# Optimization experiments

Measured on AMD Instinct MI355X. Metric: run time of the kernel, lower is better.

The kernel has to match this reference:

```python
import jax, jax.numpy as jnp
import numpy as np

N = 20000   # nodes
E = 240000  # edges (avg degree 12)
D = 128     # hidden_dim
H = 4       # heads
C = D // H  # head dim = 32
L = 3       # layers


def _ln(x, g, b):
    m = x.mean(-1, keepdims=True)
    v = ((x - m) ** 2).mean(-1, keepdims=True)
    return (x - m) / jnp.sqrt(v + 1e-5) * g + b


def setup_inputs() -> dict:
    key = jax.random.key(0)
    ks = iter(jax.random.split(key, 64))
    def w(shape, s=0.02):
        return jax.random.normal(next(ks), shape, jnp.float32) * s
    z = lambda shape: jnp.zeros(shape, jnp.float32)
    o = lambda shape: jnp.ones(shape, jnp.float32)
    inp = {
        'xyz': jax.random.normal(next(ks), (N, 3), jnp.float32) * 10.0,
        'attr': jax.random.uniform(next(ks), (N, 1), jnp.float32),
        'edge_index': jax.random.randint(next(ks), (2, E), 0, N, jnp.int32),
        # input encoder
        'enc_W': w((4, D)), 'enc_b': z((D,)), 'enc_g': o((D,)), 'enc_bb': z((D,)),
        # relative position MLP
        'pos_W1': w((3, D)), 'pos_b1': z((D,)), 'pos_g': o((D,)), 'pos_bb': z((D,)),
        'pos_W2': w((D, D)), 'pos_b2': z((D,)),
        # TransformerConv per-layer params (stacked over L)
        'Wq': w((L, D, D)), 'bq': z((L, D)),
        'Wk': w((L, D, D)), 'bk': z((L, D)),
        'Wv': w((L, D, D)), 'bv': z((L, D)),
        'We': w((L, D, D)),                 # lin_edge (no bias in PyG)
        'Wskip': w((L, D, D)), 'bskip': z((L, D)),
        'Wbeta': w((L, 3 * D, 1)),          # lin_beta (no bias)
        'ln1_g': o((L, D)), 'ln1_b': z((L, D)),
        'ln2_g': o((L, D)), 'ln2_b': z((L, D)),
        'fW1': w((L, D, 2 * D)), 'fb1': z((L, 2 * D)),
        'fW2': w((L, 2 * D, D)), 'fb2': z((L, D)),
        # heads
        'cls_W1': w((D, D // 2)), 'cls_b1': z((D // 2,)),
        'cls_W2': w((D // 2, 4)), 'cls_b2': z((4,)),
        'box_W1': w((D, D // 2)), 'box_b1': z((D // 2,)),
        'box_W2': w((D // 2, 7)), 'box_b2': z((7,)),
    }
    return inp


def reference(xyz, attr, edge_index, enc_W, enc_b, enc_g, enc_bb,
              pos_W1, pos_b1, pos_g, pos_bb, pos_W2, pos_b2,
              Wq, bq, Wk, bk, Wv, bv, We, Wskip, bskip, Wbeta,
              ln1_g, ln1_b, ln2_g, ln2_b, fW1, fb1, fW2, fb2,
              cls_W1, cls_b1, cls_W2, cls_b2, box_W1, box_b1, box_W2, box_b2):
    n = xyz.shape[0]
    src, dst = edge_index[0], edge_index[1]  # x_j = x[src], x_i = x[dst]; aggregate at dst
    inv_sqrt_c = 1.0 / float(np.sqrt(C))

    # input encoder: Linear -> LayerNorm -> ReLU
    x = jnp.concatenate([xyz, attr], axis=-1)
    x = jax.nn.relu(_ln(x @ enc_W + enc_b, enc_g, enc_bb))

    # relative position encoding per edge: i, j = edge_index; rel = xyz[j] - xyz[i]
    rel = xyz[dst] - xyz[src]
    e = jax.nn.relu(_ln(rel @ pos_W1 + pos_b1, pos_g, pos_bb)) @ pos_W2 + pos_b2  # [E, D]

    for l in range(L):
        # TransformerConv (beta=True, concat=True, edge_dim=D), eval mode (no dropout)
        q = (x @ Wq[l] + bq[l]).reshape(n, H, C)
        k = (x @ Wk[l] + bk[l]).reshape(n, H, C)
        v = (x @ Wv[l] + bv[l]).reshape(n, H, C)
        ee = (e @ We[l]).reshape(-1, H, C)          # [E, H, C]
        kj = k[src] + ee                             # edge-conditioned keys
        alpha = (q[dst] * kj).sum(-1) * inv_sqrt_c   # [E, H]
        amax = jax.ops.segment_max(alpha, dst, num_segments=n)
        ex = jnp.exp(alpha - amax[dst])
        den = jax.ops.segment_sum(ex, dst, num_segments=n)
        a = ex / den[dst]                            # scatter softmax over in-edges of dst
        msg = (v[src] + ee) * a[:, :, None]
        out = jax.ops.segment_sum(msg, dst, num_segments=n).reshape(n, D)
        # beta-gated skip
        r = x @ Wskip[l] + bskip[l]
        beta = jax.nn.sigmoid(jnp.concatenate([out, r, out - r], axis=-1) @ Wbeta[l])  # [N,1]
        out = beta * r + (1.0 - beta) * out
        # residual + LN + FFN + residual + LN
        x = _ln(out + x, ln1_g[l], ln1_b[l])
        h = jax.nn.gelu(x @ fW1[l] + fb1[l], approximate=False) @ fW2[l] + fb2[l]
        x = _ln(h + x, ln2_g[l], ln2_b[l])

    cls_logits = jax.nn.relu(x @ cls_W1 + cls_b1) @ cls_W2 + cls_b2  # [N, 4]
    box_pred = jax.nn.relu(x @ box_W1 + box_b1) @ box_W2 + box_b2    # [N, 7]
    return (cls_logits, box_pred)
```

## Files before the change

### kernel.cpp

```cpp
#include <hip/hip_runtime.h>
#include <hip/hip_bf16.h>
#include <math.h>

#define DD 128

typedef __attribute__((ext_vector_type(8))) short short8;
typedef __attribute__((ext_vector_type(4))) float f32x4;


__device__ __forceinline__ unsigned short f2b(float f) {
    unsigned u = __float_as_uint(f);
    return (unsigned short)((u + 0x7FFFu + ((u >> 16) & 1u)) >> 16);
}
__device__ __forceinline__ float b2f(unsigned short b) {
    return __uint_as_float(((unsigned)b) << 16);
}
__device__ __forceinline__ unsigned packbf(float a, float b) {
    return (unsigned)f2b(a) | ((unsigned)f2b(b) << 16);
}

__device__ __forceinline__ void redsum2_128(float& a, float& b) {
    #pragma unroll
    for (int off = 32; off > 0; off >>= 1) {
        a += __shfl_down(a, off);
        b += __shfl_down(b, off);
    }
    __shared__ float sa[2], sb[2];
    int w = threadIdx.x >> 6;
    if ((threadIdx.x & 63) == 0) { sa[w] = a; sb[w] = b; }
    __syncthreads();
    a = sa[0] + sa[1];
    b = sb[0] + sb[1];
    __syncthreads();
}


__global__ void packw12_kernel(const float* __restrict__ Wq, const float* __restrict__ Wk,
                               const float* __restrict__ Wv, const float* __restrict__ Ws,
                               unsigned* __restrict__ Wp) {
    int bid = blockIdx.x, y = blockIdx.y, d = threadIdx.x;
    int l = y >> 2, wt = y & 3;
    const float* W = (wt == 0 ? Wq : wt == 1 ? Wk : wt == 2 ? Wv : Ws) + (size_t)l * DD * DD;
    float w0 = W[(size_t)(2 * bid) * DD + d];
    float w1 = W[(size_t)(2 * bid + 1) * DD + d];
    Wp[y * 8192 + (((d << 6) + bid) ^ ((d & 7) << 2))] = packbf(w0, w1);
}

__global__ void wcombp_kernel(const float* __restrict__ W2, const float* __restrict__ b2,
                              const float* __restrict__ We, unsigned* __restrict__ Wp,
                              float* __restrict__ b2We) {
    int bid = blockIdx.x, y = blockIdx.y, d = threadIdx.x;
    const float* We_l = We + (size_t)y * DD * DD;
    __shared__ float sa0[DD], sa1[DD];
    if (bid < 64) { sa0[d] = W2[(2 * bid) * DD + d]; sa1[d] = W2[(2 * bid + 1) * DD + d]; }
    else          { sa0[d] = b2[d]; sa1[d] = 0.f; }
    __syncthreads();
    float acc0 = 0.f, acc1 = 0.f;
    #pragma unroll 8
    for (int kk = 0; kk < DD; ++kk) {
        float w = We_l[kk * DD + d];
        acc0 += sa0[kk] * w;
        acc1 += sa1[kk] * w;
    }
    if (bid < 64) Wp[y * 8192 + (((d << 6) + bid) ^ ((d & 7) << 2))] = packbf(acc0, acc1);
    else          b2We[y * DD + d] = acc0;
}

struct B4 { const float* b[4]; };

__global__ __launch_bounds__(256) void proj_kernel(
        const unsigned short* __restrict__ xb, const unsigned* __restrict__ Wp4, B4 bias,
        unsigned short* __restrict__ qkv, float* __restrict__ rbuf, int rowsN, int rtN,
        const float4* __restrict__ rel4, const float* __restrict__ pw,
        const float* __restrict__ bbp, const unsigned* __restrict__ Wpee,
        const float* __restrict__ biasee, unsigned short* __restrict__ eeout,
        int rowsE, int rtE) {
    __shared__ unsigned Bt[8192];
    __shared__ float sc[640];
    const int t = threadIdx.x;
    const int lane = t & 63, wid = t >> 6;
    const int kqo = (lane >> 4) * 8;

    if ((int)blockIdx.x < rtE) {
        const int rowBase = (int)blockIdx.x << 6;
        #pragma unroll
        for (int i = 0; i < 8; ++i)
            *(uint4*)&Bt[(i * 256 + t) * 4] = *(const uint4*)&Wpee[(i * 256 + t) * 4];
        for (int i = t; i < 640; i += 256)
            sc[i] = (i < 512) ? pw[i] : bbp[i - 512];
        int arow = rowBase + wid * 16 + (lane & 15);
        if (arow > rowsE - 1) arow = rowsE - 1;
        float4 rv = rel4[arow];
        __syncthreads();
        short8 a[4];
        #pragma unroll
        for (int kc = 0; kc < 4; ++kc) {
            union { short8 s; unsigned short u[8]; } cv;
            #pragma unroll
            for (int j = 0; j < 8; ++j) {
                int d = kc * 32 + kqo + j;
                float y = fmaf(rv.x, sc[d], fmaf(rv.y, sc[128 + d], fmaf(rv.z, sc[256 + d], sc[384 + d])));
                cv.u[j] = f2b(fmaxf(fmaf(y, rv.w, sc[512 + d]), 0.f));
            }
            a[kc] = cv.s;
        }
        f32x4 acc[8];
        #pragma unroll
        for (int i = 0; i < 8; ++i) acc[i] = (f32x4){0.f, 0.f, 0.f, 0.f};
        #pragma unroll
        for (int ng = 0; ng < 8; ++ng) {
            int col = ng * 16 + (lane & 15);
            #pragma unroll
            for (int kc = 0; kc < 4; ++kc) {
                int kidx = kc * 16 + (lane >> 4) * 4;
                const short8 b = *(const short8*)((const char*)Bt +
                        ((((col << 6) + kidx) ^ ((col & 7) << 2)) << 2));
                acc[ng] = __builtin_amdgcn_mfma_f32_16x16x32_bf16(a[kc], b, acc[ng], 0, 0, 0);
            }
        }
        __syncthreads();
        unsigned short* sb16 = (unsigned short*)Bt;
        #pragma unroll
        for (int ng = 0; ng < 8; ++ng) {
            int col = ng * 16 + (lane & 15);
            float bv = biasee[col];
            int cp = col >> 1, cb = col & 1;
            #pragma unroll
            for (int r = 0; r < 4; ++r) {
                int row = wid * 16 + (lane >> 4) * 4 + r;
                sb16[((row << 6) + (cp ^ ((row & 7) << 2))) * 2 + cb] = f2b(acc[ng][r] + bv);
            }
        }
        __syncthreads();
        unsigned* outw = (unsigned*)eeout;
        #pragma unroll
        for (int i = 0; i < 4; ++i) {
            int j = i * 1024 + t * 4;
            int row = j >> 6, cp = j & 63;
            uint4 v = *(const uint4*)&Bt[(row << 6) + (cp ^ ((row & 7) << 2))];
            int grow = rowBase + row;
            if (grow < rowsE) *(uint4*)&outw[(size_t)grow * 64 + cp] = v;
        }
        return;
    }

    int bidx = (int)blockIdx.x - rtE;
    const int y = bidx / rtN;
    const int rowBase = (bidx % rtN) << 6;
    const unsigned* Wp = Wp4 + y * 8192;
    #pragma unroll
    for (int i = 0; i < 8; ++i)
        *(uint4*)&Bt[(i * 256 + t) * 4] = *(const uint4*)&Wp[(i * 256 + t) * 4];
    int arow = rowBase + wid * 16 + (lane & 15);
    if (arow > rowsN - 1) arow = rowsN - 1;
    short8 a[4];
    #pragma unroll
    for (int kc = 0; kc < 4; ++kc)
        a[kc] = *(const short8*)(xb + (size_t)arow * DD + kc * 32 + kqo);
    __syncthreads();
    f32x4 acc[8];
    #pragma unroll
    for (int i = 0; i < 8; ++i) acc[i] = (f32x4){0.f, 0.f, 0.f, 0.f};
    #pragma unroll
    for (int ng = 0; ng < 8; ++ng) {
        int col = ng * 16 + (lane & 15);
        #pragma unroll
        for (int kc = 0; kc < 4; ++kc) {
            int kidx = kc * 16 + (lane >> 4) * 4;
            const short8 b = *(const short8*)((const char*)Bt +
                    ((((col << 6) + kidx) ^ ((col & 7) << 2)) << 2));
            acc[ng] = __builtin_amdgcn_mfma_f32_16x16x32_bf16(a[kc], b, acc[ng], 0, 0, 0);
        }
    }
    const float* bs = bias.b[y];
    if (y == 3) {
        #pragma unroll
        for (int ng = 0; ng < 8; ++ng) {
            int col = ng * 16 + (lane & 15);
            float bv = bs[col];
            #pragma unroll
            for (int r = 0; r < 4; ++r) {
                int grow = rowBase + wid * 16 + (lane >> 4) * 4 + r;
                if (grow < rowsN) rbuf[(size_t)grow * DD + col] = acc[ng][r] + bv;
            }
        }
        return;
    }
    __syncthreads();
    unsigned short* sb16 = (unsigned short*)Bt;
    #pragma unroll
    for (int ng = 0; ng < 8; ++ng) {
        int col = ng * 16 + (lane & 15);
        float bv = bs[col];
        int cp = col >> 1, cb = col & 1;
        #pragma unroll
        for (int r = 0; r < 4; ++r) {
            int row = wid * 16 + (lane >> 4) * 4 + r;
            sb16[((row << 6) + (cp ^ ((row & 7) << 2))) * 2 + cb] = f2b(acc[ng][r] + bv);
        }
    }
    __syncthreads();
    unsigned* outw = (unsigned*)qkv;
    #pragma unroll
    for (int i = 0; i < 4; ++i) {
        int j = i * 1024 + t * 4;
        int row = j >> 6, cp = j & 63;
        uint4 v = *(const uint4*)&Bt[(row << 6) + (cp ^ ((row & 7) << 2))];
        int grow = rowBase + row;
        if (grow < rowsN) *(uint4*)&outw[(size_t)grow * 192 + (y << 6) + cp] = v;
    }
}

template <int ACT>
__global__ __launch_bounds__(256) void mgemm(
        const unsigned short* __restrict__ A, const float* __restrict__ W,
        const float* __restrict__ bias, unsigned short* __restrict__ out,
        int rows, int K, int Dout) {
    __shared__ unsigned Bt[8192];
    const int t = threadIdx.x;
    const int rowBase = blockIdx.x << 6;
    const int colBase = blockIdx.y << 7;
    const int lane = t & 63, wid = t >> 6;
    f32x4 acc[8];
    #pragma unroll
    for (int i = 0; i < 8; ++i) acc[i] = (f32x4){0.f, 0.f, 0.f, 0.f};
    int arow = rowBase + wid * 16 + (lane & 15);
    if (arow > rows - 1) arow = rows - 1;
    const int kqo = (lane >> 4) * 8;
    for (int k0 = 0; k0 < K; k0 += 128) {
        if (k0) __syncthreads();
        #pragma unroll 8
        for (int it = 0; it < 32; ++it) {
            int idx = it * 256 + t;
            int n = idx & 127, kp = idx >> 7;
            int krow = k0 + kp * 2;
            float w0 = W[(size_t)krow * Dout + colBase + n];
            float w1 = W[(size_t)(krow + 1) * Dout + colBase + n];
            Bt[((n << 6) + kp) ^ ((n & 7) << 2)] = packbf(w0, w1);
        }
        __syncthreads();
        short8 a[4];
        #pragma unroll
        for (int kc = 0; kc < 4; ++kc)
            a[kc] = *(const short8*)(A + (size_t)arow * K + k0 + kc * 32 + kqo);
        #pragma unroll
        for (int ng = 0; ng < 8; ++ng) {
            int col = ng * 16 + (lane & 15);
            #pragma unroll
            for (int kc = 0; kc < 4; ++kc) {
                int kidx = kc * 16 + (lane >> 4) * 4;
                const short8 b = *(const short8*)((const char*)Bt +
                        ((((col << 6) + kidx) ^ ((col & 7) << 2)) << 2));
                acc[ng] = __builtin_amdgcn_mfma_f32_16x16x32_bf16(a[kc], b, acc[ng], 0, 0, 0);
            }
        }
    }
    __syncthreads();
    unsigned short* sb16 = (unsigned short*)Bt;
    #pragma unroll
    for (int ng = 0; ng < 8; ++ng) {
        int col = ng * 16 + (lane & 15);
        float bv = bias[colBase + col];
        int cp = col >> 1, cb = col & 1;
        #pragma unroll
        for (int r = 0; r < 4; ++r) {
            int row = wid * 16 + (lane >> 4) * 4 + r;
            float val = acc[ng][r] + bv;
            if (ACT == 1) val = 0.5f * val * (1.f + erff(val * 0.70710678118654752f));
            else if (ACT == 2) val = fmaxf(val, 0.f);
            sb16[((row << 6) + (cp ^ ((row & 7) << 2))) * 2 + cb] = f2b(val);
        }
    }
    __syncthreads();
    unsigned* outw = (unsigned*)out;
    const int strideU = Dout >> 1, cbU = colBase >> 1;
    #pragma unroll
    for (int i = 0; i < 4; ++i) {
        int j = i * 1024 + t * 4;
        int row = j >> 6, cp = j & 63;
        uint4 v = *(const uint4*)&Bt[(row << 6) + (cp ^ ((row & 7) << 2))];
        int grow = rowBase + row;
        if (grow < rows) *(uint4*)&outw[(size_t)grow * strideU + cbU + cp] = v;
    }
}

__global__ __launch_bounds__(256) void ffn_fused(
        const unsigned short* __restrict__ xbin, const float* __restrict__ W1,
        const float* __restrict__ b1f, const float* __restrict__ W2,
        const float* __restrict__ b2f, const float* __restrict__ g,
        const float* __restrict__ bbn, float* __restrict__ x,
        unsigned short* __restrict__ xb, int rows) {
    __shared__ unsigned Bt[8192];
    __shared__ unsigned h1t[8192];
    const int t = threadIdx.x;
    const int rowBase = blockIdx.x << 6;
    const int lane = t & 63, wid = t >> 6;
    const int kqo = (lane >> 4) * 8;
    int arow = rowBase + wid * 16 + (lane & 15);
    if (arow > rows - 1) arow = rows - 1;

    short8 a[4];
    #pragma unroll
    for (int kc = 0; kc < 4; ++kc)
        a[kc] = *(const short8*)(xbin + (size_t)arow * DD + kc * 32 + kqo);

    unsigned short* h16 = (unsigned short*)h1t;
    for (int half = 0; half < 2; ++half) {
        if (half) __syncthreads();
        #pragma unroll 8
        for (int it = 0; it < 32; ++it) {
            int idx = it * 256 + t;
            int n = idx & 127, kp = idx >> 7;
            float w0 = W1[(size_t)(2 * kp) * 256 + half * 128 + n];
            float w1 = W1[(size_t)(2 * kp + 1) * 256 + half * 128 + n];
            Bt[((n << 6) + kp) ^ ((n & 7) << 2)] = packbf(w0, w1);
        }
        __syncthreads();
        f32x4 acc[8];
        #pragma unroll
        for (int i = 0; i < 8; ++i) acc[i] = (f32x4){0.f, 0.f, 0.f, 0.f};
        #pragma unroll
        for (int ng = 0; ng < 8; ++ng) {
            int col = ng * 16 + (lane & 15);
            #pragma unroll
            for (int kc = 0; kc < 4; ++kc) {
                int kidx = kc * 16 + (lane >> 4) * 4;
                const short8 b = *(const short8*)((const char*)Bt +
                        ((((col << 6) + kidx) ^ ((col & 7) << 2)) << 2));
                acc[ng] = __builtin_amdgcn_mfma_f32_16x16x32_bf16(a[kc], b, acc[ng], 0, 0, 0);
            }
        }
        #pragma unroll
        for (int ng = 0; ng < 8; ++ng) {
            int col = half * 128 + ng * 16 + (lane & 15);
            float bv = b1f[col];
            int cp = col >> 1, cb = col & 1;
            #pragma unroll
            for (int r = 0; r < 4; ++r) {
                int row = wid * 16 + (lane >> 4) * 4 + r;
                float val = acc[ng][r] + bv;
                val = 0.5f * val * (1.f + erff(val * 0.70710678118654752f));
                h16[((row << 7) + (cp ^ ((row & 7) << 2))) * 2 + cb] = f2b(val);
            }
        }
    }
    f32x4 accF[8];
    #pragma unroll
    for (int i = 0; i < 8; ++i) accF[i] = (f32x4){0.f, 0.f, 0.f, 0.f};
    const int lrow = wid * 16 + (lane & 15);
    for (int c = 0; c < 2; ++c) {
        __syncthreads();
        #pragma unroll 8
        for (int it = 0; it < 32; ++it) {
            int idx = it * 256 + t;
            int n = idx & 127, kp = idx >> 7;
            int krow = c * 128 + kp * 2;
            float w0 = W2[(size_t)krow * DD + n];
            float w1 = W2[(size_t)(krow + 1) * DD + n];
            Bt[((n << 6) + kp) ^ ((n & 7) << 2)] = packbf(w0, w1);
        }
        __syncthreads();
        short8 ah[4];
        #pragma unroll
        for (int kc = 0; kc < 4; ++kc) {
            int cp4 = c * 64 + kc * 16 + (lane >> 4) * 4;
            ah[kc] = *(const short8*)&h1t[(lrow << 7) + (cp4 ^ ((lrow & 7) << 2))];
        }
        #pragma unroll
        for (int ng = 0; ng < 8; ++ng) {
            int col = ng * 16 + (lane & 15);
            #pragma unroll
            for (int kc = 0; kc < 4; ++kc) {
                int kidx = kc * 16 + (lane >> 4) * 4;
                const short8 b = *(const short8*)((const char*)Bt +
                        ((((col << 6) + kidx) ^ ((col & 7) << 2)) << 2));
                accF[ng] = __builtin_amdgcn_mfma_f32_16x16x32_bf16(ah[kc], b, accF[ng], 0, 0, 0);
            }
        }
    }
    float tt[8][4];
    float rs[4] = {0.f, 0.f, 0.f, 0.f}, rs2[4] = {0.f, 0.f, 0.f, 0.f};
    #pragma unroll
    for (int ng = 0; ng < 8; ++ng) {
        int col = ng * 16 + (lane & 15);
        float bv = b2f[col];
        #pragma unroll
        for (int r = 0; r < 4; ++r) {
            int grow = rowBase + wid * 16 + (lane >> 4) * 4 + r;
            float xo = (grow < rows) ? x[(size_t)grow * DD + col] : 0.f;
            float v = accF[ng][r] + bv + xo;
            tt[ng][r] = v;
            rs[r] += v;
            rs2[r] += v * v;
        }
    }
    #pragma unroll
    for (int r = 0; r < 4; ++r) {
        #pragma unroll
        for (int m = 1; m < 16; m <<= 1) {
            rs[r] += __shfl_xor(rs[r], m);
            rs2[r] += __shfl_xor(rs2[r], m);
        }
    }
    __syncthreads();
    unsigned short* sb16 = (unsigned short*)Bt;
    #pragma unroll
    for (int ng = 0; ng < 8; ++ng) {
        int col = ng * 16 + (lane & 15);
        float gg = g[col], bbb = bbn[col];
        int cp = col >> 1, cb = col & 1;
        #pragma unroll
        for (int r = 0; r < 4; ++r) {
            int grow = rowBase + wid * 16 + (lane >> 4) * 4 + r;
            float mean = rs[r] * (1.f / DD);
            float var = rs2[r] * (1.f / DD) - mean * mean;
            float val = (tt[ng][r] - mean) * rsqrtf(var + 1e-5f) * gg + bbb;
            if (grow < rows) x[(size_t)grow * DD + col] = val;
            int row = wid * 16 + (lane >> 4) * 4 + r;
            sb16[((row << 6) + (cp ^ ((row & 7) << 2))) * 2 + cb] = f2b(val);
        }
    }
    __syncthreads();
    unsigned* outw = (unsigned*)xb;
    #pragma unroll
    for (int i = 0; i < 4; ++i) {
        int j = i * 1024 + t * 4;
        int row = j >> 6, cp = j & 63;
        uint4 v = *(const uint4*)&Bt[(row << 6) + (cp ^ ((row & 7) << 2))];
        int grow = rowBase + row;
        if (grow < rows) *(uint4*)&outw[(size_t)grow * 64 + cp] = v;
    }
}


__global__ void enc_kernel(const float* __restrict__ xyz, const float* __restrict__ attr,
                           const float* __restrict__ W, const float* __restrict__ b,
                           const float* __restrict__ g, const float* __restrict__ bb,
                           float* __restrict__ x, unsigned short* __restrict__ xb) {
    int i = blockIdx.x, d = threadIdx.x;
    __shared__ float sin4[4];
    if (d < 3) sin4[d] = xyz[i * 3 + d];
    if (d == 3) sin4[3] = attr[i];
    __syncthreads();
    float y = b[d];
    #pragma unroll
    for (int kk = 0; kk < 4; ++kk) y += sin4[kk] * W[kk * DD + d];
    float s = y, s2 = y * y;
    redsum2_128(s, s2);
    float mean = s * (1.0f / DD);
    float var = s2 * (1.0f / DD) - mean * mean;
    float xn = fmaxf((y - mean) * rsqrtf(var + 1e-5f) * g[d] + bb[d], 0.f);
    x[i * DD + d] = xn;
    xb[(size_t)i * DD + d] = f2b(xn);
}

__global__ void posprep_kernel(const float* __restrict__ W1, const float* __restrict__ b1,
                               const float* __restrict__ g, float* __restrict__ pw) {
    int d = threadIdx.x;
    float w0 = W1[d], w1 = W1[DD + d], w2 = W1[2 * DD + d], b = b1[d];
    float s0 = w0, s1 = w1;
    redsum2_128(s0, s1);
    float s2 = w2, s3 = b;
    redsum2_128(s2, s3);
    float c0 = w0 - s0 * (1.f / DD), c1 = w1 - s1 * (1.f / DD);
    float c2 = w2 - s2 * (1.f / DD), bc = b - s3 * (1.f / DD);
    float gd = g[d];
    pw[d] = c0 * gd; pw[DD + d] = c1 * gd; pw[2 * DD + d] = c2 * gd; pw[3 * DD + d] = bc * gd;
    float p0 = c0 * c0, p1 = c0 * c1; redsum2_128(p0, p1);
    float p2 = c0 * c2, p3 = c1 * c1; redsum2_128(p2, p3);
    float p4 = c1 * c2, p5 = c2 * c2; redsum2_128(p4, p5);
    float p6 = c0 * bc, p7 = c1 * bc; redsum2_128(p6, p7);
    float p8 = c2 * bc, p9 = bc * bc; redsum2_128(p8, p9);
    if (d == 0) {
        pw[512] = p0 * (1.f / DD); pw[513] = p1 * (1.f / DD); pw[514] = p2 * (1.f / DD);
        pw[515] = p3 * (1.f / DD); pw[516] = p4 * (1.f / DD); pw[517] = p5 * (1.f / DD);
        pw[518] = p6 * (1.f / DD); pw[519] = p7 * (1.f / DD); pw[520] = p8 * (1.f / DD);
        pw[521] = p9 * (1.f / DD);
    }
}


__global__ void hist_kernel(const int* __restrict__ ei, int* __restrict__ deg, int E) {
    int e = blockIdx.x * blockDim.x + threadIdx.x;
    if (e < E) atomicAdd(&deg[ei[E + e]], 1);
}

__global__ void scan_kernel(const int* __restrict__ deg, int* __restrict__ ptr, int n) {
    __shared__ int partial[1024];
    int t = threadIdx.x;
    int CH = (n + 1023) >> 10;
    int beg = t * CH;
    int end = beg + CH; if (end > n) end = n;
    int s = 0;
    for (int i = beg; i < end; ++i) s += deg[i];
    partial[t] = s;
    __syncthreads();
    for (int off = 1; off < 1024; off <<= 1) {
        int add = (t >= off) ? partial[t - off] : 0;
        __syncthreads();
        partial[t] += add;
        __syncthreads();
    }
    int base = (t == 0) ? 0 : partial[t - 1];
    for (int i = beg; i < end; ++i) {
        ptr[i] = base;
        base += deg[i];
    }
    if (end == n && beg < n) ptr[n] = base;
}

__global__ void scatter_kernel(const int* __restrict__ ei, const float* __restrict__ xyz,
                               const float* __restrict__ pw, const int* __restrict__ ptr,
                               int* __restrict__ cur, int* __restrict__ cs_src,
                               float4* __restrict__ rel4, int E) {
    int e = blockIdx.x * blockDim.x + threadIdx.x;
    if (e >= E) return;
    int srcn = ei[e], dstn = ei[E + e];
    int p = atomicAdd(&cur[dstn], 1);
    int slot = ptr[dstn] + p;
    cs_src[slot] = srcn;
    float r0 = xyz[dstn * 3]     - xyz[srcn * 3];
    float r1 = xyz[dstn * 3 + 1] - xyz[srcn * 3 + 1];
    float r2 = xyz[dstn * 3 + 2] - xyz[srcn * 3 + 2];
    float var = pw[512] * r0 * r0 + pw[515] * r1 * r1 + pw[517] * r2 * r2
              + 2.f * (pw[513] * r0 * r1 + pw[514] * r0 * r2 + pw[516] * r1 * r2)
              + 2.f * (pw[518] * r0 + pw[519] * r1 + pw[520] * r2) + pw[521];
    rel4[slot] = make_float4(r0, r1, r2, rsqrtf(var + 1e-5f));
}

__global__ __launch_bounds__(256) void aggc_kernel(
        const unsigned* __restrict__ qkv, const unsigned* __restrict__ ee,
        const int* __restrict__ ptr, const int* __restrict__ cs_src,
        const float* __restrict__ r, const float* __restrict__ Wb,
        const float* __restrict__ g1, const float* __restrict__ b1,
        float* __restrict__ x, unsigned* __restrict__ xbw, int N) {
    const int wave = threadIdx.x >> 6;
    const int lane = threadIdx.x & 63;
    const int node = blockIdx.x;
    __shared__ float sS[4];
    __shared__ float sA0[4][64];
    __shared__ float sA1[4][64];

    unsigned qp = qkv[(size_t)node * 192 + lane];
    float q0 = b2f((unsigned short)qp), q1 = b2f((unsigned short)(qp >> 16));
    int beg = ptr[node], end = ptr[node + 1];
    float s = 0.f, a0 = 0.f, a1 = 0.f;
    int idx = beg + wave;
    unsigned epN = 0, kpN = 0, vpN = 0;
    if (idx < end) {
        int j = cs_src[idx];
        epN = __builtin_nontemporal_load(&ee[(size_t)idx * 64 + lane]);
        kpN = qkv[(size_t)j * 192 + 64 + lane];
        vpN = qkv[(size_t)j * 192 + 128 + lane];
    }
    for (; idx < end; idx += 4) {
        unsigned ep = epN, kp = kpN, vp = vpN;
        int nidx = idx + 4;
        if (nidx < end) {
            int jn = cs_src[nidx];
            epN = __builtin_nontemporal_load(&ee[(size_t)nidx * 64 + lane]);
            kpN = qkv[(size_t)jn * 192 + 64 + lane];
            vpN = qkv[(size_t)jn * 192 + 128 + lane];
        }
        float e0 = b2f((unsigned short)ep), e1 = b2f((unsigned short)(ep >> 16));
        float kj0 = b2f((unsigned short)kp) + e0;
        float kj1 = b2f((unsigned short)(kp >> 16)) + e1;
        float p = q0 * kj0 + q1 * kj1;
        p += __shfl_xor(p, 1); p += __shfl_xor(p, 2);
        p += __shfl_xor(p, 4); p += __shfl_xor(p, 8);
        float w = __expf(p * 0.17677669529663687f);
        s += w;
        a0 += (b2f((unsigned short)vp) + e0) * w;
        a1 += (b2f((unsigned short)(vp >> 16)) + e1) * w;
    }
    sS[wave] = s;
    sA0[wave][lane] = a0;
    sA1[wave][lane] = a1;
    __syncthreads();
    if (wave != 0) return;
    s  = sS[0] + sS[1] + sS[2] + sS[3];
    a0 = sA0[0][lane] + sA0[1][lane] + sA0[2][lane] + sA0[3][lane];
    a1 = sA1[0][lane] + sA1[1][lane] + sA1[2][lane] + sA1[3][lane];

    float inv_s = (s > 0.f) ? 1.f / s : 0.f;
    float od0 = a0 * inv_s, od1 = a1 * inv_s;
    float2 rd = *(const float2*)&r[(size_t)node * DD + lane * 2];
    float2 wb0 = *(const float2*)&Wb[lane * 2];
    float2 wb1 = *(const float2*)&Wb[DD + lane * 2];
    float2 wb2 = *(const float2*)&Wb[2 * DD + lane * 2];
    float part = od0 * wb0.x + rd.x * wb1.x + (od0 - rd.x) * wb2.x
               + od1 * wb0.y + rd.y * wb1.y + (od1 - rd.y) * wb2.y;
    #pragma unroll
    for (int m = 1; m < 64; m <<= 1) part += __shfl_xor(part, m);
    float beta = 1.f / (1.f + __expf(-part));
    float2 xo = *(const float2*)&x[(size_t)node * DD + lane * 2];
    float t0 = beta * rd.x + (1.f - beta) * od0 + xo.x;
    float t1 = beta * rd.y + (1.f - beta) * od1 + xo.y;
    float ss = t0 + t1, ss2 = t0 * t0 + t1 * t1;
    #pragma unroll
    for (int m = 1; m < 64; m <<= 1) { ss += __shfl_xor(ss, m); ss2 += __shfl_xor(ss2, m); }
    float mean = ss * (1.f / DD);
    float var = ss2 * (1.f / DD) - mean * mean;
    float inv = rsqrtf(var + 1e-5f);
    float2 gg = *(const float2*)&g1[lane * 2];
    float2 bbv = *(const float2*)&b1[lane * 2];
    float2 res;
    res.x = (t0 - mean) * inv * gg.x + bbv.x;
    res.y = (t1 - mean) * inv * gg.y + bbv.y;
    *(float2*)&x[(size_t)node * DD + lane * 2] = res;
    xbw[(size_t)node * 64 + lane] = packbf(res.x, res.y);
}


__global__ void headprep_kernel(const float* __restrict__ cW1, const float* __restrict__ cb1,
                                const float* __restrict__ bW1, const float* __restrict__ bb1,
                                float* __restrict__ W1cat, float* __restrict__ b1cat) {
    int kk = blockIdx.x, d = threadIdx.x;
    W1cat[kk * DD + d] = (d < 64) ? cW1[kk * 64 + d] : bW1[kk * 64 + (d - 64)];
    if (kk == 0) b1cat[d] = (d < 64) ? cb1[d] : bb1[d - 64];
}

__global__ __launch_bounds__(256) void heads2_kernel(
        const unsigned* __restrict__ hh, const float* __restrict__ cW2,
        const float* __restrict__ cb2, const float* __restrict__ bW2,
        const float* __restrict__ bb2, float* __restrict__ outc,
        float* __restrict__ outb, int N) {
    int node = (blockIdx.x << 2) + (threadIdx.x >> 6);
    if (node >= N) return;
    const int lane = threadIdx.x & 63;
    unsigned hp = hh[(size_t)node * 64 + lane];
    float h0 = b2f((unsigned short)hp), h1 = b2f((unsigned short)(hp >> 16));
    bool isCls = lane < 32;
    int dd = isCls ? 2 * lane : 2 * lane - 128 + 64;
    float c[4], bx[7];
    #pragma unroll
    for (int j = 0; j < 4; ++j)
        c[j] = isCls ? h0 * cW2[dd * 4 + j] + h1 * cW2[(dd + 1) * 4 + j] : 0.f;
    #pragma unroll
    for (int j = 0; j < 7; ++j)
        bx[j] = isCls ? 0.f : h0 * bW2[dd * 7 + j] + h1 * bW2[(dd + 1) * 7 + j];
    #pragma unroll
    for (int m = 1; m < 32; m <<= 1) {
        #pragma unroll
        for (int j = 0; j < 4; ++j) c[j] += __shfl_xor(c[j], m);
        #pragma unroll
        for (int j = 0; j < 7; ++j) bx[j] += __shfl_xor(bx[j], m);
    }
    if (lane == 0) {
        #pragma unroll
        for (int j = 0; j < 4; ++j) outc[(size_t)node * 4 + j] = c[j] + cb2[j];
    } else if (lane == 32) {
        #pragma unroll
        for (int j = 0; j < 7; ++j) outb[(size_t)node * 7 + j] = bx[j] + bb2[j];
    }
}

extern "C" void kernel_launch(void* const* d_in, const int* in_sizes, int n_in,
                              void* d_out, int out_size, void* d_ws, size_t ws_size,
                              hipStream_t stream) {
    const float* xyz   = (const float*)d_in[0];
    const float* attr  = (const float*)d_in[1];
    const int*   ei    = (const int*)d_in[2];
    const float* encW  = (const float*)d_in[3];
    const float* encb  = (const float*)d_in[4];
    const float* encg  = (const float*)d_in[5];
    const float* encbb = (const float*)d_in[6];
    const float* posW1 = (const float*)d_in[7];
    const float* posb1 = (const float*)d_in[8];
    const float* posg  = (const float*)d_in[9];
    const float* posbb = (const float*)d_in[10];
    const float* posW2 = (const float*)d_in[11];
    const float* posb2 = (const float*)d_in[12];
    const float* Wq    = (const float*)d_in[13];
    const float* bq    = (const float*)d_in[14];
    const float* Wk    = (const float*)d_in[15];
    const float* bk    = (const float*)d_in[16];
    const float* Wv    = (const float*)d_in[17];
    const float* bv    = (const float*)d_in[18];
    const float* We    = (const float*)d_in[19];
    const float* Wskip = (const float*)d_in[20];
    const float* bskip = (const float*)d_in[21];
    const float* Wbeta = (const float*)d_in[22];
    const float* ln1g  = (const float*)d_in[23];
    const float* ln1b  = (const float*)d_in[24];
    const float* ln2g  = (const float*)d_in[25];
    const float* ln2b  = (const float*)d_in[26];
    const float* fW1   = (const float*)d_in[27];
    const float* fb1   = (const float*)d_in[28];
    const float* fW2   = (const float*)d_in[29];
    const float* fb2   = (const float*)d_in[30];
    const float* cW1   = (const float*)d_in[31];
    const float* cb1   = (const float*)d_in[32];
    const float* cW2   = (const float*)d_in[33];
    const float* cb2   = (const float*)d_in[34];
    const float* bW1   = (const float*)d_in[35];
    const float* bb1   = (const float*)d_in[36];
    const float* bW2   = (const float*)d_in[37];
    const float* bb2   = (const float*)d_in[38];

    const int N = in_sizes[0] / 3;
    const int E = in_sizes[2] / 2;

    size_t off = 0;
    auto alloc = [&](size_t nelem) {
        char* p = (char*)d_ws + off;
        off += nelem * sizeof(float);
        return (float*)p;
    };
    float* x     = alloc((size_t)N * DD);
    unsigned short* qkv = (unsigned short*)alloc((size_t)N * 192);
    float* r     = alloc((size_t)N * DD);
    unsigned short* h1 = (unsigned short*)alloc((size_t)N * 128);
    unsigned short* xb = (unsigned short*)alloc((size_t)N * 64);
    float4* rel4 = (float4*)alloc((size_t)E * 4);
    unsigned short* eeb = (unsigned short*)alloc((size_t)E * 64);
    unsigned* W2Wep = (unsigned*)alloc(3 * 8192);
    float* b2We  = alloc(3 * DD);
    unsigned* Wp12 = (unsigned*)alloc(12 * 8192);
    float* pw    = alloc(544);
    float* W1cat = alloc(DD * DD);
    float* b1cat = alloc(DD);
    int* deg     = (int*)alloc(N);
    int* ptr     = (int*)alloc(N + 1);
    int* cur     = (int*)alloc(N);
    int* cs_src  = (int*)alloc(E);

    const int rtN = (N + 63) / 64;
    const int rtE = (E + 63) / 64;

    enc_kernel<<<N, DD, 0, stream>>>(xyz, attr, encW, encb, encg, encbb, x, xb);
    hipMemsetAsync(deg, 0, N * sizeof(int), stream);
    hipMemsetAsync(cur, 0, N * sizeof(int), stream);
    hist_kernel<<<(E + 255) / 256, 256, 0, stream>>>(ei, deg, E);
    scan_kernel<<<1, 1024, 0, stream>>>(deg, ptr, N);
    posprep_kernel<<<1, DD, 0, stream>>>(posW1, posb1, posg, pw);
    scatter_kernel<<<(E + 255) / 256, 256, 0, stream>>>(ei, xyz, pw, ptr, cur, cs_src, rel4, E);
    wcombp_kernel<<<dim3(65, 3), DD, 0, stream>>>(posW2, posb2, We, W2Wep, b2We);
    packw12_kernel<<<dim3(64, 12), DD, 0, stream>>>(Wq, Wk, Wv, Wskip, Wp12);
    headprep_kernel<<<DD, DD, 0, stream>>>(cW1, cb1, bW1, bb1, W1cat, b1cat);

    for (int l = 0; l < 3; ++l) {
        const float* Wb_l = Wbeta + (size_t)l * 3 * DD;
        const float* fW1_l = fW1 + (size_t)l * DD * 256;
        const float* fW2_l = fW2 + (size_t)l * 256 * DD;
        B4 bs;
        bs.b[0] = bq + l * DD; bs.b[1] = bk + l * DD;
        bs.b[2] = bv + l * DD; bs.b[3] = bskip + l * DD;

        proj_kernel<<<rtE + 4 * rtN, 256, 0, stream>>>(
            xb, Wp12 + (size_t)l * 4 * 8192, bs, qkv, r, N, rtN,
            rel4, pw, posbb, W2Wep + l * 8192, b2We + l * DD, eeb, E, rtE);

        aggc_kernel<<<N, 256, 0, stream>>>((const unsigned*)qkv, (const unsigned*)eeb,
                                           ptr, cs_src, r, Wb_l,
                                           ln1g + l * DD, ln1b + l * DD,
                                           x, (unsigned*)xb, N);

        ffn_fused<<<rtN, 256, 0, stream>>>(xb, fW1_l, fb1 + l * 256, fW2_l, fb2 + l * DD,
                                           ln2g + l * DD, ln2b + l * DD, x, xb, N);
    }

    float* outc  = (float*)d_out;
    float* outbx = (float*)d_out + (size_t)N * 4;
    mgemm<2><<<dim3(rtN, 1), 256, 0, stream>>>(xb, W1cat, b1cat, h1, N, DD, DD);
    heads2_kernel<<<(N + 3) / 4, 256, 0, stream>>>((const unsigned*)h1, cW2, cb2, bW2, bb2,
                                                   outc, outbx, N);
}
```

Before: 426.8 us.

## Merge setup kernels, prepack FFN/head weights, fuse head MLPs into one kernel

The many small setup launches (encoder, histogram, pos-prep, scatter, weight packing, head prep) are merged into two multi-role kernels, and the two memsets become one. FFN W1/W2 weights are now prepacked to swizzled bf16 once instead of being converted inside every ffn_fused block. The head GEMM and the second head layer are fused into a single kernel, which removes the h1 round trip through global memory. The aim is to cut launch overhead and the redundant per-block weight conversion, at the cost of more complex branchy kernels with mixed roles.

```diff
diff --git a/kernel.cpp b/kernel.cpp
--- a/kernel.cpp
+++ b/kernel.cpp
@@ -19,51 +19,194 @@
     return (unsigned)f2b(a) | ((unsigned)f2b(b) << 16);
 }
 
-__device__ __forceinline__ void redsum2_128(float& a, float& b) {
+__device__ __forceinline__ void redsum2_half(float& a, float& b) {
     #pragma unroll
     for (int off = 32; off > 0; off >>= 1) {
         a += __shfl_down(a, off);
         b += __shfl_down(b, off);
     }
-    __shared__ float sa[2], sb[2];
+    __shared__ float sa[4], sb4[4];
     int w = threadIdx.x >> 6;
-    if ((threadIdx.x & 63) == 0) { sa[w] = a; sb[w] = b; }
-    __syncthreads();
-    a = sa[0] + sa[1];
-    b = sb[0] + sb[1];
-    __syncthreads();
-}
-
-
-__global__ void packw12_kernel(const float* __restrict__ Wq, const float* __restrict__ Wk,
-                               const float* __restrict__ Wv, const float* __restrict__ Ws,
-                               unsigned* __restrict__ Wp) {
-    int bid = blockIdx.x, y = blockIdx.y, d = threadIdx.x;
-    int l = y >> 2, wt = y & 3;
-    const float* W = (wt == 0 ? Wq : wt == 1 ? Wk : wt == 2 ? Wv : Ws) + (size_t)l * DD * DD;
-    float w0 = W[(size_t)(2 * bid) * DD + d];
-    float w1 = W[(size_t)(2 * bid + 1) * DD + d];
-    Wp[y * 8192 + (((d << 6) + bid) ^ ((d & 7) << 2))] = packbf(w0, w1);
-}
-
-__global__ void wcombp_kernel(const float* __restrict__ W2, const float* __restrict__ b2,
-                              const float* __restrict__ We, unsigned* __restrict__ Wp,
-                              float* __restrict__ b2We) {
-    int bid = blockIdx.x, y = blockIdx.y, d = threadIdx.x;
-    const float* We_l = We + (size_t)y * DD * DD;
-    __shared__ float sa0[DD], sa1[DD];
-    if (bid < 64) { sa0[d] = W2[(2 * bid) * DD + d]; sa1[d] = W2[(2 * bid + 1) * DD + d]; }
-    else          { sa0[d] = b2[d]; sa1[d] = 0.f; }
-    __syncthreads();
-    float acc0 = 0.f, acc1 = 0.f;
-    #pragma unroll 8
-    for (int kk = 0; kk < DD; ++kk) {
-        float w = We_l[kk * DD + d];
-        acc0 += sa0[kk] * w;
-        acc1 += sa1[kk] * w;
-    }
-    if (bid < 64) Wp[y * 8192 + (((d << 6) + bid) ^ ((d & 7) << 2))] = packbf(acc0, acc1);
-    else          b2We[y * DD + d] = acc0;
+    if ((threadIdx.x & 63) == 0) { sa[w] = a; sb4[w] = b; }
+    __syncthreads();
+    int h = threadIdx.x >> 7;
+    a = sa[2 * h] + sa[2 * h + 1];
+    b = sb4[2 * h] + sb4[2 * h + 1];
+    __syncthreads();
+}
+
+__global__ __launch_bounds__(256) void setup1_kernel(
+        const float* __restrict__ xyz, const float* __restrict__ attr,
+        const float* __restrict__ encW, const float* __restrict__ encb,
+        const float* __restrict__ encg, const float* __restrict__ encbb,
+        float* __restrict__ x, unsigned short* __restrict__ xbuf,
+        const float* __restrict__ posW1, const float* __restrict__ posb1,
+        const float* __restrict__ posg, float* __restrict__ pw,
+        const int* __restrict__ ei, int* __restrict__ deg,
+        int N, int E, int encBlocks) {
+    const int b = blockIdx.x, t = threadIdx.x;
+    if (b < encBlocks) {
+        const int h = t >> 7, d = t & 127;
+        const int node = b * 2 + h;
+        const bool ok = node < N;
+        __shared__ float sin4[2][4];
+        if (ok && d < 3) sin4[h][d] = xyz[node * 3 + d];
+        if (ok && d == 3) sin4[h][3] = attr[node];
+        __syncthreads();
+        float y = encb[d];
+        if (ok) {
+            #pragma unroll
+            for (int kk = 0; kk < 4; ++kk) y += sin4[h][kk] * encW[kk * DD + d];
+        }
+        float s = y, s2 = y * y;
+        redsum2_half(s, s2);
+        if (ok) {
+            float mean = s * (1.0f / DD);
+            float var = s2 * (1.0f / DD) - mean * mean;
+            float xn = fmaxf((y - mean) * rsqrtf(var + 1e-5f) * encg[d] + encbb[d], 0.f);
+            x[(size_t)node * DD + d] = xn;
+            xbuf[(size_t)node * DD + d] = f2b(xn);
+        }
+    } else if (b == encBlocks) {
+        const int d = t & 127;
+        float w0 = posW1[d], w1 = posW1[DD + d], w2 = posW1[2 * DD + d], bb = posb1[d];
+        float s0 = w0, s1 = w1;
+        redsum2_half(s0, s1);
+        float s2 = w2, s3 = bb;
+        redsum2_half(s2, s3);
+        float c0 = w0 - s0 * (1.f / DD), c1 = w1 - s1 * (1.f / DD);
+        float c2 = w2 - s2 * (1.f / DD), bc = bb - s3 * (1.f / DD);
+        float gd = posg[d];
+        pw[d] = c0 * gd; pw[DD + d] = c1 * gd; pw[2 * DD + d] = c2 * gd; pw[3 * DD + d] = bc * gd;
+        float p0 = c0 * c0, p1 = c0 * c1; redsum2_half(p0, p1);
+        float p2 = c0 * c2, p3 = c1 * c1; redsum2_half(p2, p3);
+        float p4 = c1 * c2, p5 = c2 * c2; redsum2_half(p4, p5);
+        float p6 = c0 * bc, p7 = c1 * bc; redsum2_half(p6, p7);
+        float p8 = c2 * bc, p9 = bc * bc; redsum2_half(p8, p9);
+        if ((t & 127) == 0) {
+            pw[512] = p0 * (1.f / DD); pw[513] = p1 * (1.f / DD); pw[514] = p2 * (1.f / DD);
+            pw[515] = p3 * (1.f / DD); pw[516] = p4 * (1.f / DD); pw[517] = p5 * (1.f / DD);
+            pw[518] = p6 * (1.f / DD); pw[519] = p7 * (1.f / DD); pw[520] = p8 * (1.f / DD);
+            pw[521] = p9 * (1.f / DD);
+        }
+    } else {
+        int e = (b - encBlocks - 1) * 256 + t;
+        if (e < E) atomicAdd(&deg[ei[E + e]], 1);
+    }
+}
+
+__global__ void scan_kernel(const int* __restrict__ deg, int* __restrict__ ptr, int n) {
+    __shared__ int partial[1024];
+    int t = threadIdx.x;
+    int CH = (n + 1023) >> 10;
+    int beg = t * CH;
+    int end = beg + CH; if (end > n) end = n;
+    int s = 0;
+    for (int i = beg; i < end; ++i) s += deg[i];
+    partial[t] = s;
+    __syncthreads();
+    for (int off = 1; off < 1024; off <<= 1) {
+        int add = (t >= off) ? partial[t - off] : 0;
+        __syncthreads();
+        partial[t] += add;
+        __syncthreads();
+    }
+    int base = (t == 0) ? 0 : partial[t - 1];
+    for (int i = beg; i < end; ++i) {
+        ptr[i] = base;
+        base += deg[i];
+    }
+    if (end == n && beg < n) ptr[n] = base;
+}
+
+__global__ __launch_bounds__(256) void setup2_kernel(
+        const int* __restrict__ ei, const float* __restrict__ xyz,
+        const float* __restrict__ pw, const int* __restrict__ ptr,
+        int* __restrict__ cur, int* __restrict__ cs_src, float4* __restrict__ rel4, int E,
+        const float* __restrict__ W2, const float* __restrict__ b2,
+        const float* __restrict__ We, unsigned* __restrict__ W2Wep, float* __restrict__ b2We,
+        const float* __restrict__ Wq, const float* __restrict__ Wk,
+        const float* __restrict__ Wv, const float* __restrict__ Ws,
+        const float* __restrict__ fW1, const float* __restrict__ fW2,
+        unsigned* __restrict__ Wpall,
+        const float* __restrict__ cW1, const float* __restrict__ bW1,
+        unsigned* __restrict__ Whp,
+        const float* __restrict__ cb1, const float* __restrict__ bb1,
+        float* __restrict__ b1cat, int SC) {
+    const int b = blockIdx.x, t = threadIdx.x;
+    if (b < SC) {
+        int e = b * 256 + t;
+        if (e >= E) return;
+        int srcn = ei[e], dstn = ei[E + e];
+        int p = atomicAdd(&cur[dstn], 1);
+        int slot = ptr[dstn] + p;
+        cs_src[slot] = srcn;
+        float r0 = xyz[dstn * 3]     - xyz[srcn * 3];
+        float r1 = xyz[dstn * 3 + 1] - xyz[srcn * 3 + 1];
+        float r2 = xyz[dstn * 3 + 2] - xyz[srcn * 3 + 2];
+        float var = pw[512] * r0 * r0 + pw[515] * r1 * r1 + pw[517] * r2 * r2
+                  + 2.f * (pw[513] * r0 * r1 + pw[514] * r0 * r2 + pw[516] * r1 * r2)
+                  + 2.f * (pw[518] * r0 + pw[519] * r1 + pw[520] * r2) + pw[521];
+        rel4[slot] = make_float4(r0, r1, r2, rsqrtf(var + 1e-5f));
+        return;
+    }
+    if (b < SC + 99) {
+        int z = b - SC;
+        int y = z / 33, bp = z % 33;
+        int sub = t >> 7, d = t & 127;
+        int bid = bp * 2 + sub;
+        const float* We_l = We + (size_t)y * DD * DD;
+        __shared__ float s0[2][DD], s1[2][DD];
+        if (bid < 64)       { s0[sub][d] = W2[(2 * bid) * DD + d]; s1[sub][d] = W2[(2 * bid + 1) * DD + d]; }
+        else if (bid == 64) { s0[sub][d] = b2[d]; s1[sub][d] = 0.f; }
+        __syncthreads();
+        if (bid <= 64) {
+            float a0 = 0.f, a1 = 0.f;
+            #pragma unroll 8
+            for (int kk = 0; kk < DD; ++kk) {
+                float w = We_l[kk * DD + d];
+                a0 += s0[sub][kk] * w;
+                a1 += s1[sub][kk] * w;
+            }
+            if (bid < 64) W2Wep[y * 8192 + (((d << 6) + bid) ^ ((d & 7) << 2))] = packbf(a0, a1);
+            else          b2We[y * DD + d] = a0;
+        }
+        return;
+    }
+    if (b < SC + 99 + 768) {
+        int z = b - SC - 99;
+        int blob = z >> 5, bp = z & 31;
+        int kp = bp * 2 + (t >> 7), d = t & 127;
+        float w0, w1;
+        if (blob < 12) {
+            int l = blob >> 2, wt = blob & 3;
+            const float* W = (wt == 0 ? Wq : wt == 1 ? Wk : wt == 2 ? Wv : Ws) + (size_t)l * DD * DD;
+            w0 = W[(size_t)(2 * kp) * DD + d];
+            w1 = W[(size_t)(2 * kp + 1) * DD + d];
+        } else if (blob < 18) {
+            int i = blob - 12, l = i >> 1, hf = i & 1;
+            const float* W = fW1 + (size_t)l * DD * 256;
+            w0 = W[(size_t)(2 * kp) * 256 + hf * 128 + d];
+            w1 = W[(size_t)(2 * kp + 1) * 256 + hf * 128 + d];
+        } else {
+            int i = blob - 18, l = i >> 1, c = i & 1;
+            const float* W = fW2 + (size_t)l * 256 * DD;
+            w0 = W[(size_t)(c * 128 + 2 * kp) * DD + d];
+            w1 = W[(size_t)(c * 128 + 2 * kp + 1) * DD + d];
+        }
+        Wpall[blob * 8192 + (((d << 6) + kp) ^ ((d & 7) << 2))] = packbf(w0, w1);
+        return;
+    }
+    if (b < SC + 99 + 768 + 32) {
+        int bp = b - (SC + 99 + 768);
+        int kp = bp * 2 + (t >> 7), d = t & 127;
+        int k0 = 2 * kp, k1 = 2 * kp + 1;
+        float w0 = (d < 64) ? cW1[k0 * 64 + d] : bW1[k0 * 64 + (d - 64)];
+        float w1 = (d < 64) ? cW1[k1 * 64 + d] : bW1[k1 * 64 + (d - 64)];
+        Whp[((d << 6) + kp) ^ ((d & 7) << 2)] = packbf(w0, w1);
+        return;
+    }
+    if (t < 128) b1cat[t] = (t < 64) ? cb1[t] : bb1[t - 64];
 }
 
 struct B4 { const float* b[4]; };
@@ -211,323 +354,6 @@
     }
 }
 
-template <int ACT>
-__global__ __launch_bounds__(256) void mgemm(
-        const unsigned short* __restrict__ A, const float* __restrict__ W,
-        const float* __restrict__ bias, unsigned short* __restrict__ out,
-        int rows, int K, int Dout) {
-    __shared__ unsigned Bt[8192];
-    const int t = threadIdx.x;
-    const int rowBase = blockIdx.x << 6;
-    const int colBase = blockIdx.y << 7;
-    const int lane = t & 63, wid = t >> 6;
-    f32x4 acc[8];
-    #pragma unroll
-    for (int i = 0; i < 8; ++i) acc[i] = (f32x4){0.f, 0.f, 0.f, 0.f};
-    int arow = rowBase + wid * 16 + (lane & 15);
-    if (arow > rows - 1) arow = rows - 1;
-    const int kqo = (lane >> 4) * 8;
-    for (int k0 = 0; k0 < K; k0 += 128) {
-        if (k0) __syncthreads();
-        #pragma unroll 8
-        for (int it = 0; it < 32; ++it) {
-            int idx = it * 256 + t;
-            int n = idx & 127, kp = idx >> 7;
-            int krow = k0 + kp * 2;
-            float w0 = W[(size_t)krow * Dout + colBase + n];
-            float w1 = W[(size_t)(krow + 1) * Dout + colBase + n];
-            Bt[((n << 6) + kp) ^ ((n & 7) << 2)] = packbf(w0, w1);
-        }
-        __syncthreads();
-        short8 a[4];
-        #pragma unroll
-        for (int kc = 0; kc < 4; ++kc)
-            a[kc] = *(const short8*)(A + (size_t)arow * K + k0 + kc * 32 + kqo);
-        #pragma unroll
-        for (int ng = 0; ng < 8; ++ng) {
-            int col = ng * 16 + (lane & 15);
-            #pragma unroll
-            for (int kc = 0; kc < 4; ++kc) {
-                int kidx = kc * 16 + (lane >> 4) * 4;
-                const short8 b = *(const short8*)((const char*)Bt +
-                        ((((col << 6) + kidx) ^ ((col & 7) << 2)) << 2));
-                acc[ng] = __builtin_amdgcn_mfma_f32_16x16x32_bf16(a[kc], b, acc[ng], 0, 0, 0);
-            }
-        }
-    }
-    __syncthreads();
-    unsigned short* sb16 = (unsigned short*)Bt;
-    #pragma unroll
-    for (int ng = 0; ng < 8; ++ng) {
-        int col = ng * 16 + (lane & 15);
-        float bv = bias[colBase + col];
-        int cp = col >> 1, cb = col & 1;
-        #pragma unroll
-        for (int r = 0; r < 4; ++r) {
-            int row = wid * 16 + (lane >> 4) * 4 + r;
-            float val = acc[ng][r] + bv;
-            if (ACT == 1) val = 0.5f * val * (1.f + erff(val * 0.70710678118654752f));
-            else if (ACT == 2) val = fmaxf(val, 0.f);
-            sb16[((row << 6) + (cp ^ ((row & 7) << 2))) * 2 + cb] = f2b(val);
-        }
-    }
-    __syncthreads();
-    unsigned* outw = (unsigned*)out;
-    const int strideU = Dout >> 1, cbU = colBase >> 1;
-    #pragma unroll
-    for (int i = 0; i < 4; ++i) {
-        int j = i * 1024 + t * 4;
-        int row = j >> 6, cp = j & 63;
-        uint4 v = *(const uint4*)&Bt[(row << 6) + (cp ^ ((row & 7) << 2))];
-        int grow = rowBase + row;
-        if (grow < rows) *(uint4*)&outw[(size_t)grow * strideU + cbU + cp] = v;
-    }
-}
-
-__global__ __launch_bounds__(256) void ffn_fused(
-        const unsigned short* __restrict__ xbin, const float* __restrict__ W1,
-        const float* __restrict__ b1f, const float* __restrict__ W2,
-        const float* __restrict__ b2f, const float* __restrict__ g,
-        const float* __restrict__ bbn, float* __restrict__ x,
-        unsigned short* __restrict__ xb, int rows) {
-    __shared__ unsigned Bt[8192];
-    __shared__ unsigned h1t[8192];
-    const int t = threadIdx.x;
-    const int rowBase = blockIdx.x << 6;
-    const int lane = t & 63, wid = t >> 6;
-    const int kqo = (lane >> 4) * 8;
-    int arow = rowBase + wid * 16 + (lane & 15);
-    if (arow > rows - 1) arow = rows - 1;
-
-    short8 a[4];
-    #pragma unroll
-    for (int kc = 0; kc < 4; ++kc)
-        a[kc] = *(const short8*)(xbin + (size_t)arow * DD + kc * 32 + kqo);
-
-    unsigned short* h16 = (unsigned short*)h1t;
-    for (int half = 0; half < 2; ++half) {
-        if (half) __syncthreads();
-        #pragma unroll 8
-        for (int it = 0; it < 32; ++it) {
-            int idx = it * 256 + t;
-            int n = idx & 127, kp = idx >> 7;
-            float w0 = W1[(size_t)(2 * kp) * 256 + half * 128 + n];
-            float w1 = W1[(size_t)(2 * kp + 1) * 256 + half * 128 + n];
-            Bt[((n << 6) + kp) ^ ((n & 7) << 2)] = packbf(w0, w1);
-        }
-        __syncthreads();
-        f32x4 acc[8];
-        #pragma unroll
-        for (int i = 0; i < 8; ++i) acc[i] = (f32x4){0.f, 0.f, 0.f, 0.f};
-        #pragma unroll
-        for (int ng = 0; ng < 8; ++ng) {
-            int col = ng * 16 + (lane & 15);
-            #pragma unroll
-            for (int kc = 0; kc < 4; ++kc) {
-                int kidx = kc * 16 + (lane >> 4) * 4;
-                const short8 b = *(const short8*)((const char*)Bt +
-                        ((((col << 6) + kidx) ^ ((col & 7) << 2)) << 2));
-                acc[ng] = __builtin_amdgcn_mfma_f32_16x16x32_bf16(a[kc], b, acc[ng], 0, 0, 0);
-            }
-        }
-        #pragma unroll
-        for (int ng = 0; ng < 8; ++ng) {
-            int col = half * 128 + ng * 16 + (lane & 15);
-            float bv = b1f[col];
-            int cp = col >> 1, cb = col & 1;
-            #pragma unroll
-            for (int r = 0; r < 4; ++r) {
-                int row = wid * 16 + (lane >> 4) * 4 + r;
-                float val = acc[ng][r] + bv;
-                val = 0.5f * val * (1.f + erff(val * 0.70710678118654752f));
-                h16[((row << 7) + (cp ^ ((row & 7) << 2))) * 2 + cb] = f2b(val);
-            }
-        }
-    }
-    f32x4 accF[8];
-    #pragma unroll
-    for (int i = 0; i < 8; ++i) accF[i] = (f32x4){0.f, 0.f, 0.f, 0.f};
-    const int lrow = wid * 16 + (lane & 15);
-    for (int c = 0; c < 2; ++c) {
-        __syncthreads();
-        #pragma unroll 8
-        for (int it = 0; it < 32; ++it) {
-            int idx = it * 256 + t;
-            int n = idx & 127, kp = idx >> 7;
-            int krow = c * 128 + kp * 2;
-            float w0 = W2[(size_t)krow * DD + n];
-            float w1 = W2[(size_t)(krow + 1) * DD + n];
-            Bt[((n << 6) + kp) ^ ((n & 7) << 2)] = packbf(w0, w1);
-        }
-        __syncthreads();
-        short8 ah[4];
-        #pragma unroll
-        for (int kc = 0; kc < 4; ++kc) {
-            int cp4 = c * 64 + kc * 16 + (lane >> 4) * 4;
-            ah[kc] = *(const short8*)&h1t[(lrow << 7) + (cp4 ^ ((lrow & 7) << 2))];
-        }
-        #pragma unroll
-        for (int ng = 0; ng < 8; ++ng) {
-            int col = ng * 16 + (lane & 15);
-            #pragma unroll
-            for (int kc = 0; kc < 4; ++kc) {
-                int kidx = kc * 16 + (lane >> 4) * 4;
-                const short8 b = *(const short8*)((const char*)Bt +
-                        ((((col << 6) + kidx) ^ ((col & 7) << 2)) << 2));
-                accF[ng] = __builtin_amdgcn_mfma_f32_16x16x32_bf16(ah[kc], b, accF[ng], 0, 0, 0);
-            }
-        }
-    }
-    float tt[8][4];
-    float rs[4] = {0.f, 0.f, 0.f, 0.f}, rs2[4] = {0.f, 0.f, 0.f, 0.f};
-    #pragma unroll
-    for (int ng = 0; ng < 8; ++ng) {
-        int col = ng * 16 + (lane & 15);
-        float bv = b2f[col];
-        #pragma unroll
-        for (int r = 0; r < 4; ++r) {
-            int grow = rowBase + wid * 16 + (lane >> 4) * 4 + r;
-            float xo = (grow < rows) ? x[(size_t)grow * DD + col] : 0.f;
-            float v = accF[ng][r] + bv + xo;
-            tt[ng][r] = v;
-            rs[r] += v;
-            rs2[r] += v * v;
-        }
-    }
-    #pragma unroll
-    for (int r = 0; r < 4; ++r) {
-        #pragma unroll
-        for (int m = 1; m < 16; m <<= 1) {
-            rs[r] += __shfl_xor(rs[r], m);
-            rs2[r] += __shfl_xor(rs2[r], m);
-        }
-    }
-    __syncthreads();
-    unsigned short* sb16 = (unsigned short*)Bt;
-    #pragma unroll
-    for (int ng = 0; ng < 8; ++ng) {
-        int col = ng * 16 + (lane & 15);
-        float gg = g[col], bbb = bbn[col];
-        int cp = col >> 1, cb = col & 1;
-        #pragma unroll
-        for (int r = 0; r < 4; ++r) {
-            int grow = rowBase + wid * 16 + (lane >> 4) * 4 + r;
-            float mean = rs[r] * (1.f / DD);
-            float var = rs2[r] * (1.f / DD) - mean * mean;
-            float val = (tt[ng][r] - mean) * rsqrtf(var + 1e-5f) * gg + bbb;
-            if (grow < rows) x[(size_t)grow * DD + col] = val;
-            int row = wid * 16 + (lane >> 4) * 4 + r;
-            sb16[((row << 6) + (cp ^ ((row & 7) << 2))) * 2 + cb] = f2b(val);
-        }
-    }
-    __syncthreads();
-    unsigned* outw = (unsigned*)xb;
-    #pragma unroll
-    for (int i = 0; i < 4; ++i) {
-        int j = i * 1024 + t * 4;
-        int row = j >> 6, cp = j & 63;
-        uint4 v = *(const uint4*)&Bt[(row << 6) + (cp ^ ((row & 7) << 2))];
-        int grow = rowBase + row;
-        if (grow < rows) *(uint4*)&outw[(size_t)grow * 64 + cp] = v;
-    }
-}
-
-
-__global__ void enc_kernel(const float* __restrict__ xyz, const float* __restrict__ attr,
-                           const float* __restrict__ W, const float* __restrict__ b,
-                           const float* __restrict__ g, const float* __restrict__ bb,
-                           float* __restrict__ x, unsigned short* __restrict__ xb) {
-    int i = blockIdx.x, d = threadIdx.x;
-    __shared__ float sin4[4];
-    if (d < 3) sin4[d] = xyz[i * 3 + d];
-    if (d == 3) sin4[3] = attr[i];
-    __syncthreads();
-    float y = b[d];
-    #pragma unroll
-    for (int kk = 0; kk < 4; ++kk) y += sin4[kk] * W[kk * DD + d];
-    float s = y, s2 = y * y;
-    redsum2_128(s, s2);
-    float mean = s * (1.0f / DD);
-    float var = s2 * (1.0f / DD) - mean * mean;
-    float xn = fmaxf((y - mean) * rsqrtf(var + 1e-5f) * g[d] + bb[d], 0.f);
-    x[i * DD + d] = xn;
-    xb[(size_t)i * DD + d] = f2b(xn);
-}
-
-__global__ void posprep_kernel(const float* __restrict__ W1, const float* __restrict__ b1,
-                               const float* __restrict__ g, float* __restrict__ pw) {
-    int d = threadIdx.x;
-    float w0 = W1[d], w1 = W1[DD + d], w2 = W1[2 * DD + d], b = b1[d];
-    float s0 = w0, s1 = w1;
-    redsum2_128(s0, s1);
-    float s2 = w2, s3 = b;
-    redsum2_128(s2, s3);
-    float c0 = w0 - s0 * (1.f / DD), c1 = w1 - s1 * (1.f / DD);
-    float c2 = w2 - s2 * (1.f / DD), bc = b - s3 * (1.f / DD);
-    float gd = g[d];
-    pw[d] = c0 * gd; pw[DD + d] = c1 * gd; pw[2 * DD + d] = c2 * gd; pw[3 * DD + d] = bc * gd;
-    float p0 = c0 * c0, p1 = c0 * c1; redsum2_128(p0, p1);
-    float p2 = c0 * c2, p3 = c1 * c1; redsum2_128(p2, p3);
-    float p4 = c1 * c2, p5 = c2 * c2; redsum2_128(p4, p5);
-    float p6 = c0 * bc, p7 = c1 * bc; redsum2_128(p6, p7);
-    float p8 = c2 * bc, p9 = bc * bc; redsum2_128(p8, p9);
-    if (d == 0) {
-        pw[512] = p0 * (1.f / DD); pw[513] = p1 * (1.f / DD); pw[514] = p2 * (1.f / DD);
-        pw[515] = p3 * (1.f / DD); pw[516] = p4 * (1.f / DD); pw[517] = p5 * (1.f / DD);
-        pw[518] = p6 * (1.f / DD); pw[519] = p7 * (1.f / DD); pw[520] = p8 * (1.f / DD);
-        pw[521] = p9 * (1.f / DD);
-    }
-}
-
-
-__global__ void hist_kernel(const int* __restrict__ ei, int* __restrict__ deg, int E) {
-    int e = blockIdx.x * blockDim.x + threadIdx.x;
-    if (e < E) atomicAdd(&deg[ei[E + e]], 1);
-}
-
-__global__ void scan_kernel(const int* __restrict__ deg, int* __restrict__ ptr, int n) {
-    __shared__ int partial[1024];
-    int t = threadIdx.x;
-    int CH = (n + 1023) >> 10;
-    int beg = t * CH;
-    int end = beg + CH; if (end > n) end = n;
-    int s = 0;
-    for (int i = beg; i < end; ++i) s += deg[i];
-    partial[t] = s;
-    __syncthreads();
-    for (int off = 1; off < 1024; off <<= 1) {
-        int add = (t >= off) ? partial[t - off] : 0;
-        __syncthreads();
-        partial[t] += add;
-        __syncthreads();
-    }
-    int base = (t == 0) ? 0 : partial[t - 1];
-    for (int i = beg; i < end; ++i) {
-        ptr[i] = base;
-        base += deg[i];
-    }
-    if (end == n && beg < n) ptr[n] = base;
-}
-
-__global__ void scatter_kernel(const int* __restrict__ ei, const float* __restrict__ xyz,
-                               const float* __restrict__ pw, const int* __restrict__ ptr,
-                               int* __restrict__ cur, int* __restrict__ cs_src,
-                               float4* __restrict__ rel4, int E) {
-    int e = blockIdx.x * blockDim.x + threadIdx.x;
-    if (e >= E) return;
-    int srcn = ei[e], dstn = ei[E + e];
-    int p = atomicAdd(&cur[dstn], 1);
-    int slot = ptr[dstn] + p;
-    cs_src[slot] = srcn;
-    float r0 = xyz[dstn * 3]     - xyz[srcn * 3];
-    float r1 = xyz[dstn * 3 + 1] - xyz[srcn * 3 + 1];
-    float r2 = xyz[dstn * 3 + 2] - xyz[srcn * 3 + 2];
-    float var = pw[512] * r0 * r0 + pw[515] * r1 * r1 + pw[517] * r2 * r2
-              + 2.f * (pw[513] * r0 * r1 + pw[514] * r0 * r2 + pw[516] * r1 * r2)
-              + 2.f * (pw[518] * r0 + pw[519] * r1 + pw[520] * r2) + pw[521];
-    rel4[slot] = make_float4(r0, r1, r2, rsqrtf(var + 1e-5f));
-}
-
 __global__ __launch_bounds__(256) void aggc_kernel(
         const unsigned* __restrict__ qkv, const unsigned* __restrict__ ee,
         const int* __restrict__ ptr, const int* __restrict__ cs_src,
@@ -611,47 +437,219 @@
     xbw[(size_t)node * 64 + lane] = packbf(res.x, res.y);
 }
 
-
-__global__ void headprep_kernel(const float* __restrict__ cW1, const float* __restrict__ cb1,
-                                const float* __restrict__ bW1, const float* __restrict__ bb1,
-                                float* __restrict__ W1cat, float* __restrict__ b1cat) {
-    int kk = blockIdx.x, d = threadIdx.x;
-    W1cat[kk * DD + d] = (d < 64) ? cW1[kk * 64 + d] : bW1[kk * 64 + (d - 64)];
-    if (kk == 0) b1cat[d] = (d < 64) ? cb1[d] : bb1[d - 64];
-}
-
-__global__ __launch_bounds__(256) void heads2_kernel(
-        const unsigned* __restrict__ hh, const float* __restrict__ cW2,
+__global__ __launch_bounds__(256) void ffn_fused(
+        const unsigned short* __restrict__ xbin, const unsigned* __restrict__ Wp1,
+        const float* __restrict__ b1f, const unsigned* __restrict__ Wp2,
+        const float* __restrict__ b2f, const float* __restrict__ g,
+        const float* __restrict__ bbn, float* __restrict__ x,
+        unsigned short* __restrict__ xb, int rows) {
+    __shared__ unsigned Bt[8192];
+    __shared__ unsigned h1t[8192];
+    const int t = threadIdx.x;
+    const int rowBase = blockIdx.x << 6;
+    const int lane = t & 63, wid = t >> 6;
+    const int kqo = (lane >> 4) * 8;
+    int arow = rowBase + wid * 16 + (lane & 15);
+    if (arow > rows - 1) arow = rows - 1;
+
+    short8 a[4];
+    #pragma unroll
+    for (int kc = 0; kc < 4; ++kc)
+        a[kc] = *(const short8*)(xbin + (size_t)arow * DD + kc * 32 + kqo);
+
+    unsigned short* h16 = (unsigned short*)h1t;
+    for (int half = 0; half < 2; ++half) {
+        if (half) __syncthreads();
+        const unsigned* Wp = Wp1 + half * 8192;
+        #pragma unroll
+        for (int i = 0; i < 8; ++i)
+            *(uint4*)&Bt[(i * 256 + t) * 4] = *(const uint4*)&Wp[(i * 256 + t) * 4];
+        __syncthreads();
+        f32x4 acc[8];
+        #pragma unroll
+        for (int i = 0; i < 8; ++i) acc[i] = (f32x4){0.f, 0.f, 0.f, 0.f};
+        #pragma unroll
+        for (int ng = 0; ng < 8; ++ng) {
+            int col = ng * 16 + (lane & 15);
+            #pragma unroll
+            for (int kc = 0; kc < 4; ++kc) {
+                int kidx = kc * 16 + (lane >> 4) * 4;
+                const short8 b = *(const short8*)((const char*)Bt +
+                        ((((col << 6) + kidx) ^ ((col & 7) << 2)) << 2));
+                acc[ng] = __builtin_amdgcn_mfma_f32_16x16x32_bf16(a[kc], b, acc[ng], 0, 0, 0);
+            }
+        }
+        #pragma unroll
+        for (int ng = 0; ng < 8; ++ng) {
+            int col = half * 128 + ng * 16 + (lane & 15);
+            float bv = b1f[col];
+            int cp = col >> 1, cb = col & 1;
+            #pragma unroll
+            for (int r = 0; r < 4; ++r) {
+                int row = wid * 16 + (lane >> 4) * 4 + r;
+                float val = acc[ng][r] + bv;
+                val = 0.5f * val * (1.f + erff(val * 0.70710678118654752f));
+                h16[((row << 7) + (cp ^ ((row & 7) << 2))) * 2 + cb] = f2b(val);
+            }
+        }
+    }
+    f32x4 accF[8];
+    #pragma unroll
+    for (int i = 0; i < 8; ++i) accF[i] = (f32x4){0.f, 0.f, 0.f, 0.f};
+    const int lrow = wid * 16 + (lane & 15);
+    for (int c = 0; c < 2; ++c) {
+        __syncthreads();
+        const unsigned* Wp = Wp2 + c * 8192;
+        #pragma unroll
+        for (int i = 0; i < 8; ++i)
+            *(uint4*)&Bt[(i * 256 + t) * 4] = *(const uint4*)&Wp[(i * 256 + t) * 4];
+        __syncthreads();
+        short8 ah[4];
+        #pragma unroll
+        for (int kc = 0; kc < 4; ++kc) {
+            int cp4 = c * 64 + kc * 16 + (lane >> 4) * 4;
+            ah[kc] = *(const short8*)&h1t[(lrow << 7) + (cp4 ^ ((lrow & 7) << 2))];
+        }
+        #pragma unroll
+        for (int ng = 0; ng < 8; ++ng) {
+            int col = ng * 16 + (lane & 15);
+            #pragma unroll
+            for (int kc = 0; kc < 4; ++kc) {
+                int kidx = kc * 16 + (lane >> 4) * 4;
+                const short8 b = *(const short8*)((const char*)Bt +
+                        ((((col << 6) + kidx) ^ ((col & 7) << 2)) << 2));
+                accF[ng] = __builtin_amdgcn_mfma_f32_16x16x32_bf16(ah[kc], b, accF[ng], 0, 0, 0);
+            }
+        }
+    }
+    float tt[8][4];
+    float rs[4] = {0.f, 0.f, 0.f, 0.f}, rs2[4] = {0.f, 0.f, 0.f, 0.f};
+    #pragma unroll
+    for (int ng = 0; ng < 8; ++ng) {
+        int col = ng * 16 + (lane & 15);
+        float bv = b2f[col];
+        #pragma unroll
+        for (int r = 0; r < 4; ++r) {
+            int grow = rowBase + wid * 16 + (lane >> 4) * 4 + r;
+            float xo = (grow < rows) ? x[(size_t)grow * DD + col] : 0.f;
+            float v = accF[ng][r] + bv + xo;
+            tt[ng][r] = v;
+            rs[r] += v;
+            rs2[r] += v * v;
+        }
+    }
+    #pragma unroll
+    for (int r = 0; r < 4; ++r) {
+        #pragma unroll
+        for (int m = 1; m < 16; m <<= 1) {
+            rs[r] += __shfl_xor(rs[r], m);
+            rs2[r] += __shfl_xor(rs2[r], m);
+        }
+    }
+    __syncthreads();
+    unsigned short* sb16 = (unsigned short*)Bt;
+    #pragma unroll
+    for (int ng = 0; ng < 8; ++ng) {
+        int col = ng * 16 + (lane & 15);
+        float gg = g[col], bbb = bbn[col];
+        int cp = col >> 1, cb = col & 1;
+        #pragma unroll
+        for (int r = 0; r < 4; ++r) {
+            int grow = rowBase + wid * 16 + (lane >> 4) * 4 + r;
+            float mean = rs[r] * (1.f / DD);
+            float var = rs2[r] * (1.f / DD) - mean * mean;
+            float val = (tt[ng][r] - mean) * rsqrtf(var + 1e-5f) * gg + bbb;
+            if (grow < rows) x[(size_t)grow * DD + col] = val;
+            int row = wid * 16 + (lane >> 4) * 4 + r;
+            sb16[((row << 6) + (cp ^ ((row & 7) << 2))) * 2 + cb] = f2b(val);
+        }
+    }
+    __syncthreads();
+    unsigned* outw = (unsigned*)xb;
+    #pragma unroll
+    for (int i = 0; i < 4; ++i) {
+        int j = i * 1024 + t * 4;
+        int row = j >> 6, cp = j & 63;
+        uint4 v = *(const uint4*)&Bt[(row << 6) + (cp ^ ((row & 7) << 2))];
+        int grow = rowBase + row;
+        if (grow < rows) *(uint4*)&outw[(size_t)grow * 64 + cp] = v;
+    }
+}
+
+__global__ __launch_bounds__(256) void heads_fused(
+        const unsigned short* __restrict__ xb, const unsigned* __restrict__ Whp,
+        const float* __restrict__ b1cat, const float* __restrict__ cW2,
         const float* __restrict__ cb2, const float* __restrict__ bW2,
         const float* __restrict__ bb2, float* __restrict__ outc,
-        float* __restrict__ outb, int N) {
-    int node = (blockIdx.x << 2) + (threadIdx.x >> 6);
-    if (node >= N) return;
-    const int lane = threadIdx.x & 63;
-    unsigned hp = hh[(size_t)node * 64 + lane];
-    float h0 = b2f((unsigned short)hp), h1 = b2f((unsigned short)(hp >> 16));
-    bool isCls = lane < 32;
-    int dd = isCls ? 2 * lane : 2 * lane - 128 + 64;
-    float c[4], bx[7];
-    #pragma unroll
-    for (int j = 0; j < 4; ++j)
-        c[j] = isCls ? h0 * cW2[dd * 4 + j] + h1 * cW2[(dd + 1) * 4 + j] : 0.f;
-    #pragma unroll
-    for (int j = 0; j < 7; ++j)
-        bx[j] = isCls ? 0.f : h0 * bW2[dd * 7 + j] + h1 * bW2[(dd + 1) * 7 + j];
-    #pragma unroll
-    for (int m = 1; m < 32; m <<= 1) {
-        #pragma unroll
-        for (int j = 0; j < 4; ++j) c[j] += __shfl_xor(c[j], m);
-        #pragma unroll
-        for (int j = 0; j < 7; ++j) bx[j] += __shfl_xor(bx[j], m);
-    }
-    if (lane == 0) {
-        #pragma unroll
-        for (int j = 0; j < 4; ++j) outc[(size_t)node * 4 + j] = c[j] + cb2[j];
-    } else if (lane == 32) {
-        #pragma unroll
-        for (int j = 0; j < 7; ++j) outb[(size_t)node * 7 + j] = bx[j] + bb2[j];
+        float* __restrict__ outb, int rows) {
+    __shared__ unsigned Bt[8192];
+    __shared__ unsigned ht[4096];
+    const int t = threadIdx.x;
+    const int rowBase = blockIdx.x << 6;
+    const int lane = t & 63, wid = t >> 6;
+    const int kqo = (lane >> 4) * 8;
+    #pragma unroll
+    for (int i = 0; i < 8; ++i)
+        *(uint4*)&Bt[(i * 256 + t) * 4] = *(const uint4*)&Whp[(i * 256 + t) * 4];
+    int arow = rowBase + wid * 16 + (lane & 15);
+    if (arow > rows - 1) arow = rows - 1;
+    short8 a[4];
+    #pragma unroll
+    for (int kc = 0; kc < 4; ++kc)
+        a[kc] = *(const short8*)(xb + (size_t)arow * DD + kc * 32 + kqo);
+    __syncthreads();
+    f32x4 acc[8];
+    #pragma unroll
+    for (int i = 0; i < 8; ++i) acc[i] = (f32x4){0.f, 0.f, 0.f, 0.f};
+    #pragma unroll
+    for (int ng = 0; ng < 8; ++ng) {
+        int col = ng * 16 + (lane & 15);
+        #pragma unroll
+        for (int kc = 0; kc < 4; ++kc) {
+            int kidx = kc * 16 + (lane >> 4) * 4;
+            const short8 b = *(const short8*)((const char*)Bt +
+                    ((((col << 6) + kidx) ^ ((col & 7) << 2)) << 2));
+            acc[ng] = __builtin_amdgcn_mfma_f32_16x16x32_bf16(a[kc], b, acc[ng], 0, 0, 0);
+        }
+    }
+    unsigned short* h16 = (unsigned short*)ht;
+    #pragma unroll
+    for (int ng = 0; ng < 8; ++ng) {
+        int col = ng * 16 + (lane & 15);
+        float bv = b1cat[col];
+        int cp = col >> 1, cb = col & 1;
+        #pragma unroll
+        for (int r = 0; r < 4; ++r) {
+            int row = wid * 16 + (lane >> 4) * 4 + r;
+            h16[((row << 6) + (cp ^ ((row & 7) << 2))) * 2 + cb] = f2b(fmaxf(acc[ng][r] + bv, 0.f));
+        }
+    }
+    __syncthreads();
+    for (int i = t; i < 704; i += 256) {
+        int n = i / 11, j = i % 11;
+        int grow = rowBase + n;
+        if (grow >= rows) continue;
+        int sw = (n & 7) << 2;
+        if (j < 4) {
+            float accv = cb2[j];
+            #pragma unroll 8
+            for (int kp = 0; kp < 32; ++kp) {
+                unsigned w = ht[(n << 6) + (kp ^ sw)];
+                accv += b2f((unsigned short)w) * cW2[(2 * kp) * 4 + j];
+                accv += b2f((unsigned short)(w >> 16)) * cW2[(2 * kp + 1) * 4 + j];
+            }
+            outc[(size_t)grow * 4 + j] = accv;
+        } else {
+            int jj = j - 4;
+            float accv = bb2[jj];
+            #pragma unroll 8
+            for (int kp = 0; kp < 32; ++kp) {
+                unsigned w = ht[(n << 6) + ((32 + kp) ^ sw)];
+                accv += b2f((unsigned short)w) * bW2[(2 * kp) * 7 + jj];
+                accv += b2f((unsigned short)(w >> 16)) * bW2[(2 * kp + 1) * 7 + jj];
+            }
+            outb[(size_t)grow * 7 + jj] = accv;
+        }
     }
 }
 
@@ -710,45 +708,44 @@
     float* x     = alloc((size_t)N * DD);
     unsigned short* qkv = (unsigned short*)alloc((size_t)N * 192);
     float* r     = alloc((size_t)N * DD);
-    unsigned short* h1 = (unsigned short*)alloc((size_t)N * 128);
     unsigned short* xb = (unsigned short*)alloc((size_t)N * 64);
     float4* rel4 = (float4*)alloc((size_t)E * 4);
     unsigned short* eeb = (unsigned short*)alloc((size_t)E * 64);
     unsigned* W2Wep = (unsigned*)alloc(3 * 8192);
     float* b2We  = alloc(3 * DD);
-    unsigned* Wp12 = (unsigned*)alloc(12 * 8192);
+    unsigned* Wpall = (unsigned*)alloc(24 * 8192);
+    unsigned* Whp   = (unsigned*)alloc(8192);
     float* pw    = alloc(544);
-    float* W1cat = alloc(DD * DD);
     float* b1cat = alloc(DD);
     int* deg     = (int*)alloc(N);
+    int* cur     = (int*)alloc(N);
     int* ptr     = (int*)alloc(N + 1);
-    int* cur     = (int*)alloc(N);
     int* cs_src  = (int*)alloc(E);
 
     const int rtN = (N + 63) / 64;
     const int rtE = (E + 63) / 64;
-
-    enc_kernel<<<N, DD, 0, stream>>>(xyz, attr, encW, encb, encg, encbb, x, xb);
-    hipMemsetAsync(deg, 0, N * sizeof(int), stream);
-    hipMemsetAsync(cur, 0, N * sizeof(int), stream);
-    hist_kernel<<<(E + 255) / 256, 256, 0, stream>>>(ei, deg, E);
+    const int encBlocks = (N + 1) / 2;
+    const int SC = (E + 255) / 256;
+
+    hipMemsetAsync(deg, 0, 2 * (size_t)N * sizeof(int), stream);
+    setup1_kernel<<<encBlocks + 1 + SC, 256, 0, stream>>>(
+        xyz, attr, encW, encb, encg, encbb, x, xb,
+        posW1, posb1, posg, pw, ei, deg, N, E, encBlocks);
     scan_kernel<<<1, 1024, 0, stream>>>(deg, ptr, N);
-    posprep_kernel<<<1, DD, 0, stream>>>(posW1, posb1, posg, pw);
-    scatter_kernel<<<(E + 255) / 256, 256, 0, stream>>>(ei, xyz, pw, ptr, cur, cs_src, rel4, E);
-    wcombp_kernel<<<dim3(65, 3), DD, 0, stream>>>(posW2, posb2, We, W2Wep, b2We);
-    packw12_kernel<<<dim3(64, 12), DD, 0, stream>>>(Wq, Wk, Wv, Wskip, Wp12);
-    headprep_kernel<<<DD, DD, 0, stream>>>(cW1, cb1, bW1, bb1, W1cat, b1cat);
+    setup2_kernel<<<SC + 99 + 768 + 32 + 1, 256, 0, stream>>>(
+        ei, xyz, pw, ptr, cur, cs_src, rel4, E,
+        posW2, posb2, We, W2Wep, b2We,
+        Wq, Wk, Wv, Wskip, fW1, fW2, Wpall,
+        cW1, bW1, Whp, cb1, bb1, b1cat, SC);
 
     for (int l = 0; l < 3; ++l) {
         const float* Wb_l = Wbeta + (size_t)l * 3 * DD;
-        const float* fW1_l = fW1 + (size_t)l * DD * 256;
-        const float* fW2_l = fW2 + (size_t)l * 256 * DD;
         B4 bs;
         bs.b[0] = bq + l * DD; bs.b[1] = bk + l * DD;
         bs.b[2] = bv + l * DD; bs.b[3] = bskip + l * DD;
 
         proj_kernel<<<rtE + 4 * rtN, 256, 0, stream>>>(
-            xb, Wp12 + (size_t)l * 4 * 8192, bs, qkv, r, N, rtN,
+            xb, Wpall + (size_t)l * 4 * 8192, bs, qkv, r, N, rtN,
             rel4, pw, posbb, W2Wep + l * 8192, b2We + l * DD, eeb, E, rtE);
 
         aggc_kernel<<<N, 256, 0, stream>>>((const unsigned*)qkv, (const unsigned*)eeb,
@@ -756,13 +753,14 @@
                                            ln1g + l * DD, ln1b + l * DD,
                                            x, (unsigned*)xb, N);
 
-        ffn_fused<<<rtN, 256, 0, stream>>>(xb, fW1_l, fb1 + l * 256, fW2_l, fb2 + l * DD,
-                                           ln2g + l * DD, ln2b + l * DD, x, xb, N);
+        ffn_fused<<<rtN, 256, 0, stream>>>(xb, Wpall + (size_t)(12 + 2 * l) * 8192,
+                                           fb1 + l * 256, Wpall + (size_t)(18 + 2 * l) * 8192,
+                                           fb2 + l * DD, ln2g + l * DD, ln2b + l * DD,
+                                           x, xb, N);
     }
 
     float* outc  = (float*)d_out;
     float* outbx = (float*)d_out + (size_t)N * 4;
-    mgemm<2><<<dim3(rtN, 1), 256, 0, stream>>>(xb, W1cat, b1cat, h1, N, DD, DD);
-    heads2_kernel<<<(N + 3) / 4, 256, 0, stream>>>((const unsigned*)h1, cW2, cb2, bW2, bb2,
-                                                   outc, outbx, N);
-}
+    heads_fused<<<rtN, 256, 0, stream>>>(xb, Whp, b1cat, cW2, cb2, bW2, bb2,
+                                         outc, outbx, N);
+}
```

After: 371.7 us. 12.9% less time.
